# Performance work log

Measured on AMD Instinct MI355X. Metric: run time of the kernel, lower is better.

## Reference

```python
import jax, jax.numpy as jnp
import numpy as np

B, N, C_IN, C_EMB, G = 16, 1024, 16, 64, 128
NEG = -1e12


def _lap(m):
    # m @ D^-1/2, transpose, @ D^-1/2  (matches torch code incl. transpose)
    d = jnp.sum(m, axis=1) ** -0.5
    return (m * d[None, :]).T * d[None, :]


def setup_inputs():
    key = jax.random.key(0)
    ks = jax.random.split(key, 16)
    f = jax.random.normal
    return {
        'x': f(ks[0], (B, C_IN, N), jnp.float32),
        'ct': f(ks[1], (B, C_EMB, N), jnp.float32),
        'graph_data': jax.random.uniform(ks[2], (2, N, N), dtype=jnp.float32),
        'emb_w': f(ks[3], (C_EMB, C_IN)) / np.sqrt(C_IN).astype(np.float32),
        'emb_b': f(ks[4], (C_EMB,)) * 0.01,
        'emb2_w': f(ks[5], (N, N)) / np.sqrt(N).astype(np.float32),
        'emb2_b': f(ks[6], (N,)) * 0.01,
        'att_W': f(ks[7], (C_EMB, C_EMB)) / np.sqrt(C_EMB).astype(np.float32),
        'att_a': f(ks[8], (2 * C_EMB, 1)) / np.sqrt(2 * C_EMB).astype(np.float32),
        'att_GL': f(ks[9], (N, G)) / np.sqrt(G).astype(np.float32),
        'uai_w': f(ks[10], (C_EMB, C_EMB)) / np.sqrt(C_EMB).astype(np.float32),
        'uai_b': f(ks[11], (C_EMB,)) * 0.01,
        'lin1_w': f(ks[12], (C_EMB, C_EMB)) / np.sqrt(C_EMB).astype(np.float32),
        'lin2_w': f(ks[13], (C_EMB, C_EMB)) / np.sqrt(C_EMB).astype(np.float32),
        'lin2_b': f(ks[14], (C_EMB,)) * 0.01,
        'ln_w': jnp.ones((C_EMB, N), jnp.float32),
        'ln_b': jnp.zeros((C_EMB, N), jnp.float32),
    }


def reference(x, ct, graph_data, emb_w, emb_b, emb2_w, emb2_b, att_W, att_a,
              att_GL, uai_w, uai_b, lin1_w, lin2_w, lin2_b, ln_w, ln_b):
    # emb: Conv1d k=1 -> leaky_relu -> Linear over node axis N
    h0 = jax.nn.leaky_relu(jnp.einsum('bcn,ec->ben', x, emb_w) + emb_b[None, :, None])
    h0 = jnp.einsum('ben,mn->bem', h0, emb2_w) + emb2_b[None, None, :]
    inp = jnp.swapaxes(h0, 1, 2)  # [B,N,C']

    # InterpositionAttention (repeat/cat factorized: e_ij = leakyrelu(a1.h_i + a2.h_j))
    eye = jnp.eye(N, dtype=x.dtype)
    adj_att = jax.nn.softmax(jax.nn.relu(att_GL @ att_GL.T), axis=-1) + eye
    h = inp @ att_W  # [B,N,C']
    e = jax.nn.leaky_relu((h @ att_a[:C_EMB]) + jnp.swapaxes(h @ att_a[C_EMB:], 1, 2))  # [B,N,N]
    att = jax.nn.softmax(jnp.where(adj_att > 0, e, NEG), axis=2)
    x_att = jnp.swapaxes(jax.nn.relu(att @ h), 1, 2)  # [B,C',N]

    # UAI module (eval mode: dropout off -> all MC samples equal -> sigma = 0)
    mu = jnp.swapaxes(x_att, 1, 2) @ uai_w.T + uai_b  # [B,N,C']
    x_uai = jnp.swapaxes(mu, 1, 2)  # [B,C',N]

    g1 = _lap(graph_data[0] + eye)
    g2 = _lap(graph_data[1] + eye)

    # learned adjacency from pairwise squared distances (cdist p=2, squared)
    xf = jnp.swapaxes(x_uai, 1, 2)  # [B,N,C']
    sq = jnp.sum(xf * xf, axis=-1)
    d2 = jnp.maximum(sq[:, :, None] + sq[:, None, :] - 2.0 * (xf @ jnp.swapaxes(xf, 1, 2)), 0.0)
    gl = jax.nn.softmax(jnp.exp(-d2 / (2.0 * C_EMB)) + eye, axis=-1)  # sigma^2 = emb_size

    def ln(z):  # LayerNorm over last two dims [C', N]
        m = jnp.mean(z, axis=(1, 2), keepdims=True)
        v = jnp.var(z, axis=(1, 2), keepdims=True)
        return (z - m) / jnp.sqrt(v + 1e-5) * ln_w + ln_b

    l1 = lambda z: jnp.einsum('oc,bcn->bon', lin1_w, z)
    l2 = lambda z: jnp.einsum('oc,bcn->bon', lin2_w, z) + lin2_b[None, :, None]

    x_new = ln(l1(x_uai) @ gl + l1(l1(x_uai) @ g1) @ g2)
    ft = jax.nn.gelu(ln(l2(x_uai) @ gl + l2(l2(x_uai) @ g1) @ g2), approximate=False)
    rt = ft  # rt is computed by the identical expression (dropout off)

    ct_new = ft * ct + x_new - ft * x_new
    ht = rt * jax.nn.elu(ct_new) + x_uai - rt * x_uai
    return (ht, ct_new)
```

## Files before the change

kernel.cpp:

```cpp
#include <hip/hip_runtime.h>
#include <math.h>

typedef unsigned short u16;
typedef __attribute__((ext_vector_type(8))) short short8;
typedef __attribute__((ext_vector_type(4))) float floatx4;

constexpr int BATCH = 16;
constexpr int NI = 1024;
constexpr int CE = 64;
constexpr int CI = 16;
constexpr long long NN2  = (long long)NI * NI;
constexpr long long BCN  = (long long)BATCH * CE * NI;
constexpr long long BNv  = (long long)BATCH * NI;
constexpr long long BNN  = (long long)BATCH * NI * NI;
constexpr long long S1 = (long long)CE * NI;
constexpr long long S2 = 2 * S1;
constexpr int ZERON = (int)(2 * BNv + 80);

__device__ __forceinline__ float lrelu01(float x) { return x > 0.f ? x : 0.01f * x; }

__device__ __forceinline__ u16 f2bf(float f) {
  unsigned u = __builtin_bit_cast(unsigned, f);
  return (u16)((u + 0x7fffu + ((u >> 16) & 1u)) >> 16);
}
__device__ __forceinline__ float bf2f(u16 h) {
  unsigned u = ((unsigned)h) << 16;
  return __builtin_bit_cast(float, u);
}
__device__ __forceinline__ unsigned fkey(float f) {
  unsigned u = __builtin_bit_cast(unsigned, f);
  return (u & 0x80000000u) ? ~u : (u | 0x80000000u);
}
__device__ __forceinline__ float funkey(unsigned k) {
  unsigned u = (k & 0x80000000u) ? (k & 0x7fffffffu) : ~k;
  return __builtin_bit_cast(float, u);
}

__device__ __forceinline__ void gload16(const u16* g, u16* l) {
  __builtin_amdgcn_global_load_lds(
      (const __attribute__((address_space(1))) void*)g,
      (__attribute__((address_space(3))) void*)l, 16, 0, 0);
}

__device__ __forceinline__ void fence13() {
  __builtin_amdgcn_sched_barrier(0);
  asm volatile("s_waitcnt vmcnt(2) lgkmcnt(0)" ::: "memory");
  __builtin_amdgcn_s_barrier();
  __builtin_amdgcn_sched_barrier(0);
}

template<int N>
__device__ __forceinline__ void fence_bar() {
  __builtin_amdgcn_sched_barrier(0);
  if constexpr (N == 0) asm volatile("s_waitcnt vmcnt(0)" ::: "memory");
  else if constexpr (N == 1) asm volatile("s_waitcnt vmcnt(1)" ::: "memory");
  else if constexpr (N == 2) asm volatile("s_waitcnt vmcnt(2)" ::: "memory");
  else if constexpr (N == 3) asm volatile("s_waitcnt vmcnt(3)" ::: "memory");
  else if constexpr (N == 4) asm volatile("s_waitcnt vmcnt(4)" ::: "memory");
  else if constexpr (N == 6) asm volatile("s_waitcnt vmcnt(6)" ::: "memory");
  else asm volatile("s_waitcnt vmcnt(0)" ::: "memory");
  __builtin_amdgcn_s_barrier();
  __builtin_amdgcn_sched_barrier(0);
}

template<int BM, int BN, int MODE>
__global__ __launch_bounds__(256) void mgemm(
    const u16* __restrict__ Ag, const u16* __restrict__ B1g, const u16* __restrict__ B2g,
    int K1, int K, int lda, int ldb, long long bsA, long long bsB1,
    float* __restrict__ Cf, u16* __restrict__ Cb, int ldc, long long bsC,
    const float* __restrict__ aux1, const float* __restrict__ aux2,
    const float* __restrict__ aux3, const float* __restrict__ aux4,
    float* __restrict__ Zout)
{
  constexpr int RM = BM / 2, RN = BN / 2, MI = RM / 16, NJ = RN / 16;
  constexpr bool PIPE3 = (MODE == 5 || MODE == 14 || MODE == 15);
  constexpr int NBB = PIPE3 ? 3 : (MODE == 13 ? 3 : 1);
  constexpr int NBA = PIPE3 ? 3 : (MODE == 13 ? 2 : 1);
  constexpr int NLA = (BM * 8) / 256;
  constexpr int NLB = (BN * 8) / 256;
  constexpr int L = (NLA + NLB);
  __shared__ __align__(16) u16 As[NBA * BM * 64];
  __shared__ __align__(16) u16 Bs[NBB * BN * 64];
  __shared__ __align__(16) u16 xa[MODE == 13 ? 32 * 72 : 1];
  const int tid = threadIdx.x;
  int z, n0, r0, job15 = 0;
  bool job4 = false;
  long long cboff = 0;
  if constexpr (MODE == 15) {
    const int id = blockIdx.x;
    if (id >= 512 && id < 1536) {
      const int m = id - 512;
      float s = 0.f, sv = 0.f;
      for (int n = tid; n < NI; n += 256) {
        float g = aux3[(long long)m * NI + n] * aux2[n];
        s += g;
        sv = fmaf(g, aux1[n], sv);
      }
      float* r1 = (float*)As;
      float* r2 = (float*)As + 256;
      r1[tid] = s; r2[tid] = sv; __syncthreads();
      for (int st = 128; st > 0; st >>= 1) {
        if (tid < st) { r1[tid] += r1[tid + st]; r2[tid] += r2[tid + st]; }
        __syncthreads();
      }
      if (tid == 0) {
        float dm = aux2[m];
        Cf[m] = dm * (r1[0] + dm);
        Zout[m] = dm * (r2[0] + dm * aux1[m]);
      }
      return;
    }
    if (id >= 1536) {
      const int id2 = id - 1536;
      job15 = 2;
      z = id2 >> 5; r0 = (id2 & 1) * BM; n0 = ((id2 >> 1) & 15) * BN;
    } else {
      z = 0; n0 = (id & 15) * BN; r0 = (id >> 4) * BM;
    }
  } else if constexpr (MODE == 5) {
    const int id = blockIdx.x;
    const int xcd = id & 7, idx = id >> 3;
    z = (idx & 1) * 8 + xcd;
    r0 = 0;
    n0 = (idx >> 1) * BN;
  } else if constexpr (MODE == 3) {
    const int id = blockIdx.x;
    if (id < 4096) {
      const int xcd = id & 7, idx = id >> 3;
      z = (idx >> 8) * 8 + xcd;
      const int g = idx & 255;
      n0 = (g & 15) * 64; r0 = ((g >> 4) & 15) * 64;
    } else {
      const int t4 = id - 4096;
      job4 = true;
      z = t4 >> 6;
      const int g = t4 & 63;
      r0 = (g >> 4) * 64;
      n0 = (g & 15) * 64;
    }
  } else if constexpr (MODE == 13 || MODE == 14) {
    const int id = blockIdx.x;
    const int xcd = id & 7, idx = id >> 3;
    z = (idx >> 5) * 8 + xcd;
    if constexpr (MODE == 13) { r0 = (idx & 31) * BM; n0 = 0; }
    else { n0 = (idx & 31) * BN; r0 = 0; }
  } else {
    z = blockIdx.z; n0 = blockIdx.x * BN; r0 = blockIdx.y * BM;
  }
  int Kv = K, K1v = K1, ldav = lda, ldbv = ldb;
  const u16 *Ab, *Bb1;
  if constexpr (MODE == 15) {
    if (job15 == 2) {
      Kv = 64; K1v = 128; ldav = 64; ldbv = 64;
      Ab = B2g + (long long)r0 * 64;
      Bb1 = (const u16*)aux4 + (long long)z * S1 + (long long)n0 * 64;
      cboff = bsB1 + (long long)z * S1;
    } else {
      Ab = Ag + (long long)r0 * lda;
      Bb1 = B1g + (long long)n0 * ldb;
    }
  } else {
    Ab = Ag + (long long)z * bsA + (long long)r0 * ldav;
    Bb1 = B1g + (long long)z * bsB1 + (long long)n0 * ldbv;
    if constexpr (MODE == 3) {
      if (job4) Ab = ((const u16*)aux2) + (long long)r0 * 64;
    }
  }
  const int lane = tid & 63;
  const int wid = tid >> 6;
  const int wr = wid >> 1, wc = wid & 1;
  const int q = lane >> 4, mlow = lane & 15;
  const int wbase = tid & ~63;

  floatx4 acc[MI][NJ] = {};
  float zp0 = 0.f;

  float s1r_13 = 0.f, mr_13 = 0.f;
  const float* s2z_13 = nullptr;
  float4 sa, sb;
  if constexpr (MODE == 13) {
    const float* s1z = aux2 + (long long)z * NI;
    s2z_13 = aux3 + (long long)z * NI;
    const float mb = funkey(((const unsigned*)aux4)[z]);
    s1r_13 = s1z[r0 + (tid >> 3)];
    mr_13 = lrelu01(s1r_13 + mb);
  }

  auto stageAB = [&](int buf, int k0) {
    if constexpr (MODE != 13) {
      const u16* Asrc = Ab + k0;
#pragma unroll
      for (int s = 0; s < NLA; s++) {
        int cid = tid + s * 256;
        int r = cid >> 3, cc = cid & 7;
        gload16(Asrc + (long long)r * ldav + ((cc ^ (r & 7)) << 3),
                As + buf * (BM * 64) + ((wbase + s * 256) << 3));
      }
    }
    const u16* Bsrc = (k0 < K1v) ? (Bb1 + k0)
                                 : (B2g + (long long)n0 * ldbv + (k0 - K1v));
#pragma unroll
    for (int s = 0; s < NLB; s++) {
      int cid = tid + s * 256;
      int r = cid >> 3, cc = cid & 7;
      gload16(Bsrc + (long long)r * ldbv + ((cc ^ (r & 7)) << 3),
              Bs + buf * (BN * 64) + ((wbase + s * 256) << 3));
    }
  };

  auto agen_ld = [&](int k0) {
    const float* sp = s2z_13 + k0 + (tid & 7) * 8;
    sa = *(const float4*)sp;
    sb = *(const float4*)(sp + 4);
  };
  auto agen_st = [&](int buf) {
    int r = tid >> 3, craw = tid & 7;
    float p0 = __expf(lrelu01(s1r_13 + sa.x) - mr_13);
    float p1 = __expf(lrelu01(s1r_13 + sa.y) - mr_13);
    float p2 = __expf(lrelu01(s1r_13 + sa.z) - mr_13);
    float p3 = __expf(lrelu01(s1r_13 + sa.w) - mr_13);
    float p4 = __expf(lrelu01(s1r_13 + sb.x) - mr_13);
    float p5 = __expf(lrelu01(s1r_13 + sb.y) - mr_13);
    float p6 = __expf(lrelu01(s1r_13 + sb.z) - mr_13);
    float p7 = __expf(lrelu01(s1r_13 + sb.w) - mr_13);
    zp0 += p0 + p1 + p2 + p3 + p4 + p5 + p6 + p7;
    uint4 v;
    v.x = (unsigned)f2bf(p0) | ((unsigned)f2bf(p1) << 16);
    v.y = (unsigned)f2bf(p2) | ((unsigned)f2bf(p3) << 16);
    v.z = (unsigned)f2bf(p4) | ((unsigned)f2bf(p5) << 16);
    v.w = (unsigned)f2bf(p6) | ((unsigned)f2bf(p7) << 16);
    *(uint4*)&As[buf * (BM * 64) + (r * 8 + (craw ^ (r & 7))) * 8] = v;
  };

  auto compute_tile = [&](int bufA, int bufB) {
#pragma unroll
    for (int kh = 0; kh < 2; kh++) {
      const int kc = kh * 4 + q;
      short8 afr[MI], bfr[NJ];
#pragma unroll
      for (int i = 0; i < MI; i++) {
        int row = wr * RM + i * 16 + mlow;
        afr[i] = *(const short8*)&As[bufA * (BM * 64) + (row * 8 + (kc ^ (row & 7))) * 8];
      }
#pragma unroll
      for (int j = 0; j < NJ; j++) {
        int row = wc * RN + j * 16 + mlow;
        bfr[j] = *(const short8*)&Bs[bufB * (BN * 64) + (row * 8 + (kc ^ (row & 7))) * 8];
      }
#pragma unroll
      for (int i = 0; i < MI; i++)
#pragma unroll
        for (int j = 0; j < NJ; j++)
          acc[i][j] = __builtin_amdgcn_mfma_f32_16x16x32_bf16(afr[i], bfr[j], acc[i][j], 0, 0, 0);
    }
  };

  if constexpr (PIPE3) {
    const int nk = Kv >> 6;
#pragma unroll
    for (int p = 0; p < 2; p++) {
      int kk = (p < nk) ? p : (nk - 1);
      stageAB(p, kk << 6);
    }
    fence_bar<L>();
    int cur = 0, stg = 2;
    for (int ki = 0; ki < nk; ki++) {
      if (ki + 2 < nk) stageAB(stg, (ki + 2) << 6);
      compute_tile(cur, cur);
      if (ki + 1 < nk) {
        const int rem = nk - 1 - ki;
        const int u = (rem < 2) ? rem : 2;
        if (u == 2) fence_bar<L>();
        else fence_bar<0>();
      }
      cur++; if (cur == NBB) cur = 0;
      stg++; if (stg == NBB) stg = 0;
    }
    __syncthreads();
  } else if constexpr (MODE == 13) {
    const int nk = Kv >> 6;
    agen_ld(0);
    stageAB(0, 0);
    if (nk > 1) stageAB(1, 64);
    agen_st(0);
    fence13();
    for (int ki = 0; ki < nk; ki++) {
      if (ki + 1 < nk) agen_ld((ki + 1) << 6);
      if (ki + 2 < nk) stageAB((ki + 2) % 3, (ki + 2) << 6);
      if (ki + 1 < nk) agen_st((ki + 1) & 1);
      compute_tile(ki & 1, ki % 3);
      fence13();
    }
  } else {
    for (int k0 = 0; k0 < Kv; k0 += 64) {
      stageAB(0, k0);
      __syncthreads();
      compute_tile(0, 0);
      __syncthreads();
    }
  }

  if constexpr (MODE == 3) {
    if (job4) {
      u16* abig = (u16*)Cf;
#pragma unroll
      for (int i = 0; i < MI; i++) {
#pragma unroll
        for (int j = 0; j < NJ; j++) {
#pragma unroll
          for (int rg = 0; rg < 4; rg++) {
            int r = r0 + wr * RM + i * 16 + q * 4 + rg;
            int ncol = n0 + wc * RN + j * 16 + mlow;
            int blk = r >> 6, oo = r & 63;
            int drow = ((blk & 1) << 6) + oo;
            float v = acc[i][j][rg];
            if (blk < 2) v += aux3[drow];
            abig[(long long)z * (128 * 2048LL) + (long long)drow * 2048 +
                 (long long)(blk >> 1) * 1024 + ncol] = f2bf(v);
          }
        }
      }
    } else {
      const float* sqb = aux1 + (long long)z * NI;
#pragma unroll
      for (int i = 0; i < MI; i++) {
#pragma unroll
        for (int rg = 0; rg < 4; rg++) {
          int r = r0 + wr * RM + i * 16 + q * 4 + rg;
          float sqi = sqb[r];
          float rsum = 0.f;
#pragma unroll
          for (int j = 0; j < NJ; j++) {
            int ncol = n0 + wc * RN + j * 16 + mlow;
            float d2 = fmaxf(sqi + sqb[ncol] - 2.f * acc[i][j][rg], 0.f);
            float w = __expf(__expf(-d2 * (1.f / 128.f)) + (r == ncol ? 1.f : 0.f) - 2.f);
            Cb[(long long)z * bsC + (long long)r * ldc + ncol] = f2bf(w);
            rsum += w;
          }
          rsum += __shfl_xor(rsum, 1);
          rsum += __shfl_xor(rsum, 2);
          rsum += __shfl_xor(rsum, 4);
          rsum += __shfl_xor(rsum, 8);
          if (mlow == 0) atomicAdd(&Zout[(long long)z * NI + r], rsum);
        }
      }
    }
  } else if constexpr (MODE == 14) {
    float ps1 = 0.f, ps2 = 0.f;
#pragma unroll
    for (int i = 0; i < MI; i++) {
#pragma unroll
      for (int rg = 0; rg < 4; rg++) {
        int r = wr * RM + i * 16 + q * 4 + rg;
        int ncol = n0 + wc * RN + mlow;
        float v = acc[i][0][rg] + aux3[r] * aux1[ncol];
        Cb[(long long)z * bsC + (long long)r * ldc + ncol] = f2bf(v);
        ps1 = fmaf(v, aux2[r], ps1);
        ps2 = fmaf(v, aux2[64 + r], ps2);
      }
    }
    ps1 += __shfl_xor(ps1, 16); ps1 += __shfl_xor(ps1, 32);
    ps2 += __shfl_xor(ps2, 16); ps2 += __shfl_xor(ps2, 32);
    float* sred = (float*)As;
    const int col = wc * RN + mlow;
    if (q == 0) { sred[col * 2 + wr] = ps1; sred[64 + col * 2 + wr] = ps2; }
    __syncthreads();
    if (tid < 32) {
      float v1 = sred[tid * 2] + sred[tid * 2 + 1];
      float v2 = sred[64 + tid * 2] + sred[64 + tid * 2 + 1];
      Cf[(long long)z * NI + n0 + tid] = v1;
      Zout[(long long)z * NI + n0 + tid] = v2;
      float mx = v2;
      for (int off = 1; off < 32; off <<= 1) mx = fmaxf(mx, __shfl_xor(mx, off));
      if (tid == 0) atomicMax((unsigned*)B2g + z, fkey(mx));
    }
  } else if constexpr (MODE == 13) {
    float* zred = (float*)xa;
    float* zinv = (float*)xa + 256;
    zred[(tid >> 3) * 8 + (tid & 7)] = zp0;
    __syncthreads();
    if (tid < 32) {
      float sum = 0.f;
#pragma unroll
      for (int j = 0; j < 8; j++) sum += zred[tid * 8 + j];
      zinv[tid] = 1.f / sum;
    }
    __syncthreads();
    float zr[4];
#pragma unroll
    for (int rg = 0; rg < 4; rg++) zr[rg] = zinv[wr * 16 + q * 4 + rg];
    __syncthreads();
#pragma unroll
    for (int j = 0; j < NJ; j++) {
#pragma unroll
      for (int rg = 0; rg < 4; rg++) {
        int row = wr * 16 + q * 4 + rg;
        int col = wc * RN + j * 16 + mlow;
        float v = fmaxf(acc[0][j][rg] * zr[rg], 0.f);
        xa[row * 72 + col] = f2bf(v);
      }
    }
#pragma unroll
    for (int s = 0; s < 2; s++) {
      int cid = tid + s * 256;
      int r = cid >> 3, cc = cid & 7;
      gload16(B2g + r * 64 + ((cc ^ (r & 7)) << 3),
              Bs + ((wbase + s * 256) << 3));
    }
    __syncthreads();
    floatx4 acc2[2] = {};
#pragma unroll
    for (int kh = 0; kh < 2; kh++) {
      const int kc = kh * 4 + q;
      short8 a2 = *(const short8*)&xa[(wr * 16 + mlow) * 72 + kc * 8];
#pragma unroll
      for (int j = 0; j < 2; j++) {
        int orow = wc * 32 + j * 16 + mlow;
        short8 b2 = *(const short8*)&Bs[(orow * 8 + (kc ^ (orow & 7))) * 8];
        acc2[j] = __builtin_amdgcn_mfma_f32_16x16x32_bf16(a2, b2, acc2[j], 0, 0, 0);
      }
    }
#pragma unroll
    for (int rg = 0; rg < 4; rg++) {
      int row = r0 + wr * 16 + q * 4 + rg;
      float sqp = 0.f;
#pragma unroll
      for (int j = 0; j < 2; j++) {
        int o = wc * 32 + j * 16 + mlow;
        float v = acc2[j][rg] + aux1[o];
        Cb[(long long)z * bsC + (long long)row * ldc + o] = f2bf(v);
        sqp = fmaf(v, v, sqp);
      }
      sqp += __shfl_xor(sqp, 1);
      sqp += __shfl_xor(sqp, 2);
      sqp += __shfl_xor(sqp, 4);
      sqp += __shfl_xor(sqp, 8);
      if (mlow == 0) atomicAdd(&Zout[(long long)z * NI + row], sqp);
    }
  } else if constexpr (MODE == 5) {
    float ts = 0.f, tss = 0.f;
#pragma unroll
    for (int i = 0; i < MI; i++) {
#pragma unroll
      for (int j = 0; j < NJ; j++) {
#pragma unroll
        for (int rg = 0; rg < 4; rg++) {
          int r = wr * RM + i * 16 + q * 4 + rg;
          int ncol = n0 + wc * RN + j * 16 + mlow;
          float v = acc[i][j][rg];
          v += aux3[r] * aux1[ncol] + aux4[r] * aux2[ncol];
          Cb[(long long)z * bsC + (long long)r * ldc + ncol] = f2bf(v);
          ts += v;
          tss = fmaf(v, v, tss);
        }
      }
    }
    float* red = (float*)As;
    red[tid] = ts; red[256 + tid] = tss;
    __syncthreads();
    for (int st = 64; st > 0; st >>= 1) {
      if ((tid & 127) < st) {
        red[tid] += red[tid + st];
        red[256 + tid] += red[256 + tid + st];
      }
      __syncthreads();
    }
    if (tid == 0) {
      atomicAdd(&Zout[z * 2 + 0], red[0]);
      atomicAdd(&Zout[32 + z * 2 + 0], red[256]);
    }
    if (tid == 128) {
      atomicAdd(&Zout[z * 2 + 1], red[128]);
      atomicAdd(&Zout[32 + z * 2 + 1], red[256 + 128]);
    }
  } else {
#pragma unroll
    for (int i = 0; i < MI; i++) {
#pragma unroll
      for (int j = 0; j < NJ; j++) {
#pragma unroll
        for (int rg = 0; rg < 4; rg++) {
          int r = r0 + wr * RM + i * 16 + q * 4 + rg;
          int ncol = n0 + wc * RN + j * 16 + mlow;
          Cb[cboff + (long long)r * ldc + ncol] = f2bf(acc[i][j][rg]);
        }
      }
    }
  }
}

__global__ __launch_bounds__(256) void adiv(u16* __restrict__ abig,
                                            const float* __restrict__ Zgl)
{
  const int bid = blockIdx.x;
  const int z = bid >> 6;
  const int r = (bid & 63) * 2;
  const int t = threadIdx.x;
  const int c = t * 4;
  const float4 zv = *(const float4*)(Zgl + (long long)z * NI + c);
  const float i0 = __builtin_amdgcn_rcpf(zv.x);
  const float i1 = __builtin_amdgcn_rcpf(zv.y);
  const float i2 = __builtin_amdgcn_rcpf(zv.z);
  const float i3 = __builtin_amdgcn_rcpf(zv.w);
  u16* base = abig + (long long)z * (128 * 2048LL) + (long long)r * 2048 + c;
#pragma unroll
  for (int rr = 0; rr < 2; rr++) {
    u16* p = base + (long long)rr * 2048;
    uint2 v = *(uint2*)p;
    u16 o[4];
    o[0] = f2bf(bf2f((u16)(v.x & 0xffff)) * i0);
    o[1] = f2bf(bf2f((u16)(v.x >> 16)) * i1);
    o[2] = f2bf(bf2f((u16)(v.y & 0xffff)) * i2);
    o[3] = f2bf(bf2f((u16)(v.y >> 16)) * i3);
    *(uint2*)p = *(uint2*)o;
  }
}

__global__ __launch_bounds__(256) void lap_rowsum(const float* __restrict__ gd,
                                                  float* __restrict__ dr,
                                                  float* __restrict__ zero)
{
  if (blockIdx.x >= 2048) {
    int i = (blockIdx.x - 2048) * 256 + threadIdx.x;
    if (i < ZERON) zero[i] = 0.f;
    return;
  }
  const int ki = blockIdx.x;
  const float* row = gd + (long long)ki * NI;
  float s = 0.f;
  for (int j = threadIdx.x; j < NI; j += 256) s += row[j];
  __shared__ float red[256];
  red[threadIdx.x] = s; __syncthreads();
  for (int st = 128; st > 0; st >>= 1) {
    if (threadIdx.x < st) red[threadIdx.x] += red[threadIdx.x + st];
    __syncthreads();
  }
  if (threadIdx.x == 0) dr[ki] = rsqrtf(red[0] + 1.f);
}

__global__ __launch_bounds__(256) void mega_prep(
    const float* __restrict__ l1w, const float* __restrict__ l2w,
    const float* __restrict__ l2b, const float* __restrict__ uaiw,
    const float* __restrict__ attW,
    u16* __restrict__ stack4, float* __restrict__ rb2ext, float* __restrict__ rl2ext,
    u16* __restrict__ uaiw_bf, u16* __restrict__ attwT_bf, float* __restrict__ wcs,
    const float* __restrict__ emb2w, u16* __restrict__ emb2w_bf,
    const float* __restrict__ x, const float* __restrict__ ew,
    const float* __restrict__ eb, u16* __restrict__ h0aT,
    const float* __restrict__ gd, const float* __restrict__ dsum,
    u16* __restrict__ g2t, u16* __restrict__ g1,
    float* __restrict__ cs1)
{
  __shared__ float sm[1092];
  const int bid = blockIdx.x;
  const int t = threadIdx.x;
  if (bid < 98) {
    const int gid = bid * 256 + t;
    if (gid < 4096) {
      stack4[gid] = f2bf(l1w[gid]);
    } else if (gid < 8192) {
      stack4[gid] = f2bf(l2w[gid - 4096]);
    } else if (gid < 12288) {
      int tt = gid - 8192, o = tt >> 6, m = tt & 63;
      float s = 0.f;
      for (int c = 0; c < 64; c++) s = fmaf(l1w[o * 64 + c], l1w[c * 64 + m], s);
      stack4[gid] = f2bf(s);
    } else if (gid < 16384) {
      int tt = gid - 12288, o = tt >> 6, m = tt & 63;
      float s = 0.f;
      for (int c = 0; c < 64; c++) s = fmaf(l2w[o * 64 + c], l2w[c * 64 + m], s);
      stack4[gid] = f2bf(s);
    } else if (gid < 16512) {
      int r = gid - 16384;
      rb2ext[r] = (r < 64) ? 0.f : l2b[r - 64];
    } else if (gid < 16640) {
      int r = gid - 16512;
      float v = 0.f;
      if (r >= 64) { int o = r - 64; for (int c = 0; c < 64; c++) v = fmaf(l2w[o * 64 + c], l2b[c], v); }
      rl2ext[r] = v;
    } else if (gid < 20736) {
      uaiw_bf[gid - 16640] = f2bf(uaiw[gid - 16640]);
    } else if (gid < 24832) {
      int idx = gid - 20736;
      int c = idx >> 6, e = idx & 63;
      attwT_bf[idx] = f2bf(attW[e * 64 + c]);
    } else if (gid < 24896) {
      int c = gid - 24832;
      float s = 0.f;
      for (int e = 0; e < 64; e++) s += attW[e * 64 + c];
      wcs[c] = s;
    }
  } else if (bid < 1122) {
    const long long i = (long long)(bid - 98) * 1024 + t * 4;
    float4 v = *(const float4*)(emb2w + i);
    u16 o4[4] = {f2bf(v.x), f2bf(v.y), f2bf(v.z), f2bf(v.w)};
    *(uint2*)(emb2w_bf + i) = *(const uint2*)o4;
  } else if (bid < 1378) {
    const int sub = bid - 1122;
    const int b = sub >> 4;
    const int nc = (sub & 15) * 64;
    float* we = sm;
    float* be = sm + 1024;
    for (int i = t; i < 1024; i += 256) we[i] = ew[i];
    if (t < 64) be[t] = eb[t];
    __syncthreads();
    const int n = nc + (t >> 2);
    const int e0 = (t & 3) * 16;
    const float* xb = x + (long long)b * CI * NI + n;
    float xv[16];
#pragma unroll
    for (int c = 0; c < CI; c++) xv[c] = xb[(long long)c * NI];
    u16 out16[16];
#pragma unroll
    for (int ee = 0; ee < 16; ee++) {
      const int e = e0 + ee;
      float a = be[e];
#pragma unroll
      for (int c = 0; c < CI; c++) a = fmaf(xv[c], we[e * 16 + c], a);
      out16[ee] = f2bf(lrelu01(a));
    }
    u16* dst = h0aT + (long long)b * S1 + (long long)n * 64 + e0;
    *(uint4*)dst = *(uint4*)out16;
    *(uint4*)(dst + 8) = *(uint4*)(out16 + 8);
  } else if (bid < 2402) {
    const int m = bid - 1378;
    const int j = t * 4;
    const float* d = dsum + NI;
    float4 g = *(const float4*)(gd + NN2 + (long long)m * NI + j);
    float dm = d[m];
    float4 dj = *(const float4*)(d + j);
    u16 o4[4];
    o4[0] = f2bf((g.x + (m == j     ? 1.f : 0.f)) * dm * dj.x);
    o4[1] = f2bf((g.y + (m == j + 1 ? 1.f : 0.f)) * dm * dj.y);
    o4[2] = f2bf((g.z + (m == j + 2 ? 1.f : 0.f)) * dm * dj.z);
    o4[3] = f2bf((g.w + (m == j + 3 ? 1.f : 0.f)) * dm * dj.w);
    *(uint2*)(g2t + (long long)m * NI + j) = *(const uint2*)o4;
  } else if (bid < 3426) {
    const int sub = bid - 2402;
    const int bx = (sub & 31) * 32, by = (sub >> 5) * 32;
    const int lx = t & 31, ly = t >> 5;
    float* tile = sm;
    for (int yy = ly; yy < 32; yy += 8)
      tile[yy * 33 + lx] = gd[(long long)(by + yy) * NI + bx + lx];
    __syncthreads();
    for (int yy = ly; yy < 32; yy += 8) {
      const int i = bx + yy, j = by + lx;
      float v = (tile[lx * 33 + yy] + (i == j ? 1.f : 0.f)) * dsum[i] * dsum[j];
      g1[(long long)i * NI + j] = f2bf(v);
    }
  } else {
    const int n = bid - 3426;
    float s = 0.f;
    for (int i = t; i < NI; i += 256) s = fmaf(gd[(long long)n * NI + i], dsum[i], s);
    float* red = sm;
    red[t] = s; __syncthreads();
    for (int st = 128; st > 0; st >>= 1) {
      if (t < st) red[t] += red[t + st];
      __syncthreads();
    }
    if (t == 0) cs1[n] = dsum[n] * (red[0] + dsum[n]);
  }
}

__global__ __launch_bounds__(512) void ln_final_t(const u16* __restrict__ T,
                                                  const float* __restrict__ stats,
                                                  const float* __restrict__ lnw,
                                                  const float* __restrict__ lnb,
                                                  const float* __restrict__ ct,
                                                  const u16* __restrict__ xuT,
                                                  float* __restrict__ outp)
{
  __shared__ float xs[64 * 65];
  const int blk = blockIdx.x;
  const int b = blk >> 4;
  const int n0 = (blk & 15) << 6;
  const int t = threadIdx.x;
  const int tc = t & 63, tr = t >> 6;
#pragma unroll
  for (int i = 0; i < 8; i++) {
    int nn = i * 8 + tr;
    xs[tc * 65 + nn] = bf2f(xuT[((long long)b << 16) + (long long)(n0 + nn) * 64 + tc]);
  }
  __syncthreads();
  const float inv_n = 1.f / 65536.f;
  const float m0 = stats[b * 2] * inv_n;
  const float m1 = stats[b * 2 + 1] * inv_n;
  const float rs0 = rsqrtf(fmaxf(stats[32 + b * 2] * inv_n - m0 * m0, 0.f) + 1e-5f);
  const float rs1 = rsqrtf(fmaxf(stats[32 + b * 2 + 1] * inv_n - m1 * m1, 0.f) + 1e-5f);
#pragma unroll
  for (int j = 0; j < 8; j++) {
    const int c = j * 8 + tr;
    const int n = n0 + tc;
    const int rem = c * NI + n;
    const long long toff = (long long)b * S2 + rem;
    const float t0 = bf2f(T[toff]);
    const float t1 = bf2f(T[toff + S1]);
    const float w = lnw[rem], bb = lnb[rem];
    const float xn = (t0 - m0) * rs0 * w + bb;
    float ft = (t1 - m1) * rs1 * w + bb;
    ft = 0.5f * ft * (1.f + erff(ft * 0.70710678118654752f));
    const float u = xs[c * 65 + tc];
    const long long oidx = ((long long)b << 16) + rem;
    const float cn = fmaf(ft, ct[oidx] - xn, xn);
    const float el = cn > 0.f ? cn : expm1f(cn);
    outp[oidx] = fmaf(ft, el - u, u);
    outp[BCN + oidx] = cn;
  }
}

extern "C" void kernel_launch(void* const* d_in, const int* in_sizes, int n_in,
                              void* d_out, int out_size, void* d_ws, size_t ws_size,
                              hipStream_t stream)
{
  (void)in_sizes; (void)n_in; (void)out_size; (void)ws_size;
  const float* x      = (const float*)d_in[0];
  const float* ct     = (const float*)d_in[1];
  const float* gdata  = (const float*)d_in[2];
  const float* emb_w  = (const float*)d_in[3];
  const float* emb_b  = (const float*)d_in[4];
  const float* emb2_w = (const float*)d_in[5];
  const float* emb2_b = (const float*)d_in[6];
  const float* att_W  = (const float*)d_in[7];
  const float* att_a  = (const float*)d_in[8];
  const float* uai_w  = (const float*)d_in[10];
  const float* uai_b  = (const float*)d_in[11];
  const float* lin1_w = (const float*)d_in[12];
  const float* lin2_w = (const float*)d_in[13];
  const float* lin2_b = (const float*)d_in[14];
  const float* ln_w   = (const float*)d_in[15];
  const float* ln_b   = (const float*)d_in[16];
  float* outp = (float*)d_out;

  float* ws = (float*)d_ws;
  long long o = 0;
  auto af = [&](long long n) { float* p = ws + o; o += (n + 63) & ~63LL; return p; };
  auto au = [&](long long n) { return (u16*)af((n + 1) / 2); };

  float* s1      = af(BNv);
  float* s2      = af(BNv);
  float* dsum    = af(2 * NI);
  float* cs1v    = af(NI);
  float* cs2v    = af(NI);
  float* v2v     = af(NI);
  float* rb2ext  = af(128);
  float* rl2ext  = af(128);
  float* wcs     = af(64);
  float* zeroreg = af(ZERON);
  float* Zgl     = zeroreg;
  float* sqv     = zeroreg + BNv;
  float* stats   = zeroreg + 2 * BNv;
  unsigned* s2mU = (unsigned*)(stats + 64);
  u16* Tacc      = au(S2 * BATCH);
  u16* emb2w_bf  = au(NN2);
  u16* h0aTb     = au(S1 * BATCH);
  u16* ybf       = au(S1 * BATCH);
  u16* hTb       = au(S1 * BATCH);
  u16* xuaiTb    = au(S1 * BATCH);
  u16* g1b       = au(NN2);
  u16* g2tb      = au(NN2);
  u16* G12b      = au(NN2);
  u16* Abig      = au((long long)BATCH * 128 * 2048);
  u16* stack4    = au(256 * 64);
  u16* uaiw_bf   = au(CE * CE);
  u16* attwT_bf  = au(CE * CE);
  u16* bigW      = au(BNN);

  lap_rowsum<<<2048 + (ZERON + 255) / 256, 256, 0, stream>>>(gdata, dsum, zeroreg);

  mega_prep<<<4450, 256, 0, stream>>>(
      lin1_w, lin2_w, lin2_b, uai_w, att_W,
      stack4, rb2ext, rl2ext, uaiw_bf, attwT_bf, wcs,
      emb2_w, emb2w_bf, x, emb_w, emb_b, h0aTb,
      gdata, dsum, g2tb, g1b, cs1v);

  mgemm<32, 64, 15><<<2048, 256, 0, stream>>>(
      g2tb, g1b, attwT_bf, NI, NI, NI, NI, 0, (long long)(ybf - G12b),
      cs2v, G12b, NI, 0, cs1v, dsum + NI, gdata + NN2, (const float*)h0aTb, v2v);

  mgemm<64, 32, 14><<<512, 256, 0, stream>>>(
      ybf, emb2w_bf, (const u16*)s2mU, NI, NI, NI, NI, S1, 0,
      s1, hTb, NI, S1, emb2_b, att_a, wcs, nullptr, s2);

  mgemm<32, 64, 13><<<512, 256, 0, stream>>>(
      hTb, hTb, uaiw_bf, NI, NI, NI, NI, 0, S1,
      nullptr, xuaiTb, CE, S1, uai_b, s1, s2, (const float*)s2mU, sqv);

  mgemm<64, 64, 3><<<5120, 256, 0, stream>>>(
      xuaiTb, xuaiTb, nullptr, CE, CE, CE, CE, S1, S1,
      (float*)Abig, bigW, NI, NN2, sqv, (const float*)stack4, rb2ext, nullptr, Zgl);

  adiv<<<1024, 256, 0, stream>>>(Abig, Zgl);

  mgemm<128, 64, 5><<<256, 256, 0, stream>>>(
      Abig, bigW, G12b, NI, 2 * NI, 2048, NI, (long long)128 * 2048, NN2,
      nullptr, Tacc, NI, S2, cs2v, v2v, rb2ext, rl2ext, stats);

  ln_final_t<<<256, 512, 0, stream>>>(Tacc, stats, ln_w, ln_b, ct, xuaiTb, outp);
}
```

Baseline: 220.7 us.

## Recompute Gaussian adjacency tiles on the fly inside final GEMM instead of materializing

The mode-3 GEMM no longer writes the full B×N×N bf16 Gaussian-kernel matrix. It now only accumulates row sums. A new fused kernel recomputes each 256×64 tile of that matrix from xuai with MFMA, stores it in LDS, and consumes it directly in the A·gl product, followed by the G12 GEMM and the LN statistics. This removes roughly 32MB of write plus read traffic, at the cost of recomputing the distance GEMM and exp work and raising LDS use, which may lower occupancy.

```diff
diff --git a/kernel.cpp b/kernel.cpp
--- a/kernel.cpp
+++ b/kernel.cpp
@@ -12,7 +12,6 @@
 constexpr long long NN2  = (long long)NI * NI;
 constexpr long long BCN  = (long long)BATCH * CE * NI;
 constexpr long long BNv  = (long long)BATCH * NI;
-constexpr long long BNN  = (long long)BATCH * NI * NI;
 constexpr long long S1 = (long long)CE * NI;
 constexpr long long S2 = 2 * S1;
 constexpr int ZERON = (int)(2 * BNv + 80);
@@ -73,7 +72,7 @@
     float* __restrict__ Zout)
 {
   constexpr int RM = BM / 2, RN = BN / 2, MI = RM / 16, NJ = RN / 16;
-  constexpr bool PIPE3 = (MODE == 5 || MODE == 14 || MODE == 15);
+  constexpr bool PIPE3 = (MODE == 14 || MODE == 15);
   constexpr int NBB = PIPE3 ? 3 : (MODE == 13 ? 3 : 1);
   constexpr int NBA = PIPE3 ? 3 : (MODE == 13 ? 2 : 1);
   constexpr int NLA = (BM * 8) / 256;
@@ -117,12 +116,6 @@
     } else {
       z = 0; n0 = (id & 15) * BN; r0 = (id >> 4) * BM;
     }
-  } else if constexpr (MODE == 5) {
-    const int id = blockIdx.x;
-    const int xcd = id & 7, idx = id >> 3;
-    z = (idx & 1) * 8 + xcd;
-    r0 = 0;
-    n0 = (idx >> 1) * BN;
   } else if constexpr (MODE == 3) {
     const int id = blockIdx.x;
     if (id < 4096) {
@@ -334,7 +327,6 @@
             int ncol = n0 + wc * RN + j * 16 + mlow;
             float d2 = fmaxf(sqi + sqb[ncol] - 2.f * acc[i][j][rg], 0.f);
             float w = __expf(__expf(-d2 * (1.f / 128.f)) + (r == ncol ? 1.f : 0.f) - 2.f);
-            Cb[(long long)z * bsC + (long long)r * ldc + ncol] = f2bf(w);
             rsum += w;
           }
           rsum += __shfl_xor(rsum, 1);
@@ -437,42 +429,6 @@
       sqp += __shfl_xor(sqp, 8);
       if (mlow == 0) atomicAdd(&Zout[(long long)z * NI + row], sqp);
     }
-  } else if constexpr (MODE == 5) {
-    float ts = 0.f, tss = 0.f;
-#pragma unroll
-    for (int i = 0; i < MI; i++) {
-#pragma unroll
-      for (int j = 0; j < NJ; j++) {
-#pragma unroll
-        for (int rg = 0; rg < 4; rg++) {
-          int r = wr * RM + i * 16 + q * 4 + rg;
-          int ncol = n0 + wc * RN + j * 16 + mlow;
-          float v = acc[i][j][rg];
-          v += aux3[r] * aux1[ncol] + aux4[r] * aux2[ncol];
-          Cb[(long long)z * bsC + (long long)r * ldc + ncol] = f2bf(v);
-          ts += v;
-          tss = fmaf(v, v, tss);
-        }
-      }
-    }
-    float* red = (float*)As;
-    red[tid] = ts; red[256 + tid] = tss;
-    __syncthreads();
-    for (int st = 64; st > 0; st >>= 1) {
-      if ((tid & 127) < st) {
-        red[tid] += red[tid + st];
-        red[256 + tid] += red[256 + tid + st];
-      }
-      __syncthreads();
-    }
-    if (tid == 0) {
-      atomicAdd(&Zout[z * 2 + 0], red[0]);
-      atomicAdd(&Zout[32 + z * 2 + 0], red[256]);
-    }
-    if (tid == 128) {
-      atomicAdd(&Zout[z * 2 + 1], red[128]);
-      atomicAdd(&Zout[32 + z * 2 + 1], red[256 + 128]);
-    }
   } else {
 #pragma unroll
     for (int i = 0; i < MI; i++) {
@@ -486,6 +442,229 @@
         }
       }
     }
+  }
+}
+
+__global__ __launch_bounds__(256) void fusedT(
+    const u16* __restrict__ Abig_, const u16* __restrict__ xuT,
+    const u16* __restrict__ G12, const float* __restrict__ sqv,
+    const float* __restrict__ cs2, const float* __restrict__ v2,
+    const float* __restrict__ rb2, const float* __restrict__ rl2,
+    u16* __restrict__ Tacc, float* __restrict__ stats)
+{
+  __shared__ __align__(16) u16 pool[3 * 8192];
+  __shared__ __align__(16) u16 WB[4 * 4096];
+  __shared__ __align__(16) u16 XN[64 * 64];
+  __shared__ float SQK[256];
+  __shared__ float SQM[64];
+  const int tid = threadIdx.x;
+  const int id = blockIdx.x;
+  const int xcd = id & 7, idx = id >> 3;
+  const int z = (idx & 1) * 8 + xcd;
+  const int n0 = (idx >> 1) * 64;
+  const u16* Ab = Abig_ + (long long)z * (128 * 2048LL);
+  const u16* Xz = xuT + (long long)z * S1;
+  const float* sqz = sqv + (long long)z * NI;
+  const int lane = tid & 63, wid = tid >> 6;
+  const int wr = wid >> 1, wc = wid & 1;
+  const int q = lane >> 4, mlow = lane & 15;
+  const int wbase = tid & ~63;
+
+  floatx4 acc[4][2] = {};
+
+  {
+    const u16* src = Xz + (long long)n0 * 64;
+#pragma unroll
+    for (int s = 0; s < 2; s++) {
+      int cid = tid + s * 256;
+      int r = cid >> 3, cc = cid & 7;
+      gload16(src + r * 64 + ((cc ^ (r & 7)) << 3), XN + ((wbase + s * 256) << 3));
+    }
+    if (tid < 16) *(float4*)&SQM[tid * 4] = *(const float4*)(sqz + n0 + tid * 4);
+  }
+
+  for (int kc = 0; kc < 4; kc++) {
+    __syncthreads();
+    {
+      const u16* src = Xz + (long long)(kc * 256) * 64;
+#pragma unroll
+      for (int s = 0; s < 8; s++) {
+        int cid = tid + s * 256;
+        int r = cid >> 3, cc = cid & 7;
+        gload16(src + r * 64 + ((cc ^ (r & 7)) << 3), pool + ((wbase + s * 256) << 3));
+      }
+      if (tid < 64) *(float4*)&SQK[tid * 4] = *(const float4*)(sqz + kc * 256 + tid * 4);
+    }
+    __syncthreads();
+    floatx4 a1[4][4] = {};
+#pragma unroll
+    for (int kh = 0; kh < 2; kh++) {
+      const int c8 = kh * 4 + q;
+      short8 af[4], bfv[4];
+#pragma unroll
+      for (int i = 0; i < 4; i++) {
+        int row = wid * 64 + i * 16 + mlow;
+        af[i] = *(const short8*)&pool[(row * 8 + (c8 ^ (row & 7))) * 8];
+      }
+#pragma unroll
+      for (int j = 0; j < 4; j++) {
+        int m = j * 16 + mlow;
+        bfv[j] = *(const short8*)&XN[(m * 8 + (c8 ^ (m & 7))) * 8];
+      }
+#pragma unroll
+      for (int i = 0; i < 4; i++)
+#pragma unroll
+        for (int j = 0; j < 4; j++)
+          a1[i][j] = __builtin_amdgcn_mfma_f32_16x16x32_bf16(af[i], bfv[j], a1[i][j], 0, 0, 0);
+    }
+#pragma unroll
+    for (int i = 0; i < 4; i++) {
+#pragma unroll
+      for (int j = 0; j < 4; j++) {
+        const int k64b = i * 16 + q * 4;
+        const int m = j * 16 + mlow;
+        u16 o[4];
+#pragma unroll
+        for (int rg = 0; rg < 4; rg++) {
+          int kl = wid * 64 + k64b + rg;
+          float d2 = fmaxf(SQK[kl] + SQM[m] - 2.f * a1[i][j][rg], 0.f);
+          float w = __expf(__expf(-d2 * (1.f / 128.f)) +
+                           ((kc * 256 + kl) == (n0 + m) ? 1.f : 0.f) - 2.f);
+          o[rg] = f2bf(w);
+        }
+        *(uint2*)&WB[wid * 4096 + (m * 8 + ((k64b >> 3) ^ (m & 7))) * 8 + (k64b & 7)] =
+            *(const uint2*)o;
+      }
+    }
+    __syncthreads();
+    auto stA = [&](int s, int buf) {
+      const u16* src = Ab + kc * 256 + s * 64;
+#pragma unroll
+      for (int g = 0; g < 4; g++) {
+        int cid = tid + g * 256;
+        int r = cid >> 3, cc = cid & 7;
+        gload16(src + (long long)r * 2048 + ((cc ^ (r & 7)) << 3),
+                pool + buf * 8192 + ((wbase + g * 256) << 3));
+      }
+    };
+    auto cmp = [&](int buf, int s) {
+#pragma unroll
+      for (int kh = 0; kh < 2; kh++) {
+        const int c8 = kh * 4 + q;
+        short8 af[4], bfv[2];
+#pragma unroll
+        for (int i = 0; i < 4; i++) {
+          int row = wr * 64 + i * 16 + mlow;
+          af[i] = *(const short8*)&pool[buf * 8192 + (row * 8 + (c8 ^ (row & 7))) * 8];
+        }
+#pragma unroll
+        for (int j = 0; j < 2; j++) {
+          int m = wc * 32 + j * 16 + mlow;
+          bfv[j] = *(const short8*)&WB[s * 4096 + (m * 8 + (c8 ^ (m & 7))) * 8];
+        }
+#pragma unroll
+        for (int i = 0; i < 4; i++)
+#pragma unroll
+          for (int j = 0; j < 2; j++)
+            acc[i][j] = __builtin_amdgcn_mfma_f32_16x16x32_bf16(af[i], bfv[j], acc[i][j], 0, 0, 0);
+      }
+    };
+    stA(0, 0); stA(1, 1);
+    fence_bar<4>();
+    for (int s = 0; s < 4; s++) {
+      if (s + 2 < 4) stA(s + 2, (s + 2) % 3);
+      cmp(s % 3, s);
+      if (s < 3) {
+        if (s + 2 < 4) fence_bar<4>();
+        else fence_bar<0>();
+      }
+    }
+  }
+  __syncthreads();
+  auto stG = [&](int kt, int buf) {
+    const u16* As_ = Ab + 1024 + kt * 64;
+#pragma unroll
+    for (int g = 0; g < 4; g++) {
+      int cid = tid + g * 256;
+      int r = cid >> 3, cc = cid & 7;
+      gload16(As_ + (long long)r * 2048 + ((cc ^ (r & 7)) << 3),
+              pool + buf * 8192 + ((wbase + g * 256) << 3));
+    }
+    const u16* Bs_ = G12 + (long long)n0 * NI + kt * 64;
+#pragma unroll
+    for (int g = 0; g < 2; g++) {
+      int cid = tid + g * 256;
+      int r = cid >> 3, cc = cid & 7;
+      gload16(Bs_ + (long long)r * NI + ((cc ^ (r & 7)) << 3),
+              WB + buf * 4096 + ((wbase + g * 256) << 3));
+    }
+  };
+  auto cmpG = [&](int buf) {
+#pragma unroll
+    for (int kh = 0; kh < 2; kh++) {
+      const int c8 = kh * 4 + q;
+      short8 af[4], bfv[2];
+#pragma unroll
+      for (int i = 0; i < 4; i++) {
+        int row = wr * 64 + i * 16 + mlow;
+        af[i] = *(const short8*)&pool[buf * 8192 + (row * 8 + (c8 ^ (row & 7))) * 8];
+      }
+#pragma unroll
+      for (int j = 0; j < 2; j++) {
+        int m = wc * 32 + j * 16 + mlow;
+        bfv[j] = *(const short8*)&WB[buf * 4096 + (m * 8 + (c8 ^ (m & 7))) * 8];
+      }
+#pragma unroll
+      for (int i = 0; i < 4; i++)
+#pragma unroll
+        for (int j = 0; j < 2; j++)
+          acc[i][j] = __builtin_amdgcn_mfma_f32_16x16x32_bf16(af[i], bfv[j], acc[i][j], 0, 0, 0);
+    }
+  };
+  stG(0, 0); stG(1, 1);
+  fence_bar<6>();
+  for (int kt = 0; kt < 16; kt++) {
+    if (kt + 2 < 16) stG(kt + 2, (kt + 2) % 3);
+    cmpG(kt % 3);
+    if (kt < 15) {
+      if (kt + 2 < 16) fence_bar<6>();
+      else fence_bar<0>();
+    }
+  }
+  __syncthreads();
+  float ts = 0.f, tss = 0.f;
+#pragma unroll
+  for (int i = 0; i < 4; i++) {
+#pragma unroll
+    for (int j = 0; j < 2; j++) {
+#pragma unroll
+      for (int rg = 0; rg < 4; rg++) {
+        int r = wr * 64 + i * 16 + q * 4 + rg;
+        int ncol = n0 + wc * 32 + j * 16 + mlow;
+        float v = acc[i][j][rg] + rb2[r] * cs2[ncol] + rl2[r] * v2[ncol];
+        Tacc[(long long)z * S2 + (long long)r * NI + ncol] = f2bf(v);
+        ts += v;
+        tss = fmaf(v, v, tss);
+      }
+    }
+  }
+  float* red = (float*)pool;
+  red[tid] = ts; red[256 + tid] = tss;
+  __syncthreads();
+  for (int st = 64; st > 0; st >>= 1) {
+    if ((tid & 127) < st) {
+      red[tid] += red[tid + st];
+      red[256 + tid] += red[256 + tid + st];
+    }
+    __syncthreads();
+  }
+  if (tid == 0) {
+    atomicAdd(&stats[z * 2 + 0], red[0]);
+    atomicAdd(&stats[32 + z * 2 + 0], red[256]);
+  }
+  if (tid == 128) {
+    atomicAdd(&stats[z * 2 + 1], red[128]);
+    atomicAdd(&stats[32 + z * 2 + 1], red[256 + 128]);
   }
 }
 
@@ -763,7 +942,6 @@
   u16* stack4    = au(256 * 64);
   u16* uaiw_bf   = au(CE * CE);
   u16* attwT_bf  = au(CE * CE);
-  u16* bigW      = au(BNN);
 
   lap_rowsum<<<2048 + (ZERON + 255) / 256, 256, 0, stream>>>(gdata, dsum, zeroreg);
 
@@ -787,13 +965,12 @@
 
   mgemm<64, 64, 3><<<5120, 256, 0, stream>>>(
       xuaiTb, xuaiTb, nullptr, CE, CE, CE, CE, S1, S1,
-      (float*)Abig, bigW, NI, NN2, sqv, (const float*)stack4, rb2ext, nullptr, Zgl);
+      (float*)Abig, Tacc, NI, 0, sqv, (const float*)stack4, rb2ext, nullptr, Zgl);
 
   adiv<<<1024, 256, 0, stream>>>(Abig, Zgl);
 
-  mgemm<128, 64, 5><<<256, 256, 0, stream>>>(
-      Abig, bigW, G12b, NI, 2 * NI, 2048, NI, (long long)128 * 2048, NN2,
-      nullptr, Tacc, NI, S2, cs2v, v2v, rb2ext, rl2ext, stats);
+  fusedT<<<256, 256, 0, stream>>>(
+      Abig, xuaiTb, G12b, sqv, cs2v, v2v, rb2ext, rl2ext, Tacc, stats);
 
   ln_final_t<<<256, 512, 0, stream>>>(Tacc, stats, ln_w, ln_b, ct, xuaiTb, outp);
 }
```

Result: no change. 223.7 us (+1.4%).
